# Kernel optimization log

Hardware: AMD Instinct MI355X
Metric: run time of the kernel (lower is better)

Reference implementation:

```python
import jax, jax.numpy as jnp
import numpy as np

NEG_SLOPE = 0.01  # nn.LeakyReLU default

def leaky_relu(x):
    return jnp.where(x >= 0, x, NEG_SLOPE * x)

B, C, H, W = 256, 256, 5, 5
L = H * W          # 25 locations (h==5 so no adaptive pooling)
D = C + 1          # +1 coordinate feature
HID = 64
OUT_UNITS = 32

def setup_inputs() -> dict:
    key = jax.random.key(0)
    ks = jax.random.split(key, 9)
    def xavier(k, shape):
        fan_out, fan_in = shape
        a = np.sqrt(6.0 / (fan_in + fan_out))
        return jax.random.uniform(k, shape, jnp.float32, -a, a)
    return {
        "x_img": jax.random.normal(ks[0], (B, C, H, W), jnp.float32),
        "g0_w": xavier(ks[1], (HID, 2 * D)),
        "g0_b": jnp.zeros((HID,), jnp.float32),
        "g1_w": xavier(ks[2], (HID, HID)),
        "g1_b": jnp.zeros((HID,), jnp.float32),
        "post_w": xavier(ks[3], (HID, HID)),
        "post_b": jnp.zeros((HID,), jnp.float32),
        "out_w": xavier(ks[4], (OUT_UNITS, HID)),
        "out_b": jnp.zeros((OUT_UNITS,), jnp.float32),
        "num_step": 0,
    }

def reference(x_img, g0_w, g0_b, g1_w, g1_b, post_w, post_b, out_w, out_b, num_step):
    b, c, h, w = x_img.shape
    length = h * w
    # (b, c, h*w) -> (b, L, c)
    feats = x_img.reshape(b, c, length).transpose(0, 2, 1)
    # append coordinate index feature
    coords = jnp.broadcast_to(jnp.arange(length, dtype=x_img.dtype)[None, :, None], (b, length, 1))
    feats = jnp.concatenate([feats, coords], axis=2)          # (b, L, D)
    d = feats.shape[-1]
    # all-pairs concat: x_i varies over axis 2, x_j over axis 1 (matches torch repeat/cat order)
    x_i = jnp.broadcast_to(feats[:, None, :, :], (b, length, length, d))
    x_j = jnp.broadcast_to(feats[:, :, None, :], (b, length, length, d))
    pair = jnp.concatenate([x_i, x_j], axis=3)                 # (b, L, L, 2D)
    # per-pair MLP g
    out = leaky_relu(jnp.einsum('blmd,kd->blmk', pair, g0_w) + g0_b)
    out = leaky_relu(jnp.einsum('blmk,jk->blmj', out, g1_w) + g1_b)
    # reduce over both pair axes
    out = out.sum(axis=(1, 2))                                 # (b, HID)
    # f
    out = leaky_relu(out @ post_w.T + post_b)
    out = leaky_relu(out @ out_w.T + out_b)                    # (b, OUT_UNITS)
    return out
```

## Files before the change

### kernel.cpp

```cpp
#include <hip/hip_runtime.h>

#define NB 256
#define NC 256
#define NL 25
#define ND 257
#define NOUT 32

__device__ __forceinline__ float lrelu(float x) {
    return fmaxf(x, 0.0f) + 0.01f * fminf(x, 0.0f);
}

__global__ void k_transpose(const float* __restrict__ g0, float* __restrict__ wt) {
    __shared__ float tile[64][65];
    const int cbase = blockIdx.x * 64;
    const int jh = blockIdx.y;
    const int tid = threadIdx.x;
    for (int i = tid; i < 64 * 64; i += 256) {
        int r = i >> 6, cc = i & 63, c = cbase + cc;
        float v = 0.0f;
        if (c < ND) v = g0[r * (2 * ND) + jh * ND + c];
        tile[r][cc] = v;
    }
    __syncthreads();
    for (int i = tid; i < 64 * 64; i += 256) {
        int cc = i >> 6, r = i & 63, c = cbase + cc;
        if (c < ND) wt[c * 128 + jh * 64 + r] = tile[r][cc];
    }
}

__global__ __launch_bounds__(512, 4)
void k_main(const float* __restrict__ x_img,
            const float* __restrict__ wt,
            const float* __restrict__ g0_b,
            const float* __restrict__ g1_w,
            const float* __restrict__ g1_b,
            const float* __restrict__ post_w,
            const float* __restrict__ post_b,
            const float* __restrict__ out_w,
            const float* __restrict__ out_b,
            float* __restrict__ out)
{
    __shared__ __align__(16) float xsu[6400];
    __shared__ __align__(16) float Pb[6400];
    __shared__ __align__(16) float b0s[64];
    float* xs  = xsu;
    float* uvl = xsu;
    float* red = xsu + 3200;
    float* zs  = xsu + 3520;
    float* sf  = xsu + 3584;

    const int tid  = threadIdx.x;
    const int b    = blockIdx.x;
    const int lane = tid & 63;
    const int wid  = tid >> 6;

    {
        const float4* src = (const float4*)(x_img + (size_t)b * (NC * NL));
        float4* dst = (float4*)xs;
        for (int i = tid; i < 1600; i += 512) dst[i] = src[i];
    }
    if (tid < 64) b0s[tid] = g0_b[tid];
    __syncthreads();

    {
        const int r     = tid & 255;
        const int chalf = tid >> 8;
        const int k4    = r & 15;
        const int uv    = (r >> 4) & 1;
        const int pgrp  = r >> 5;
        const int pstart = pgrp * 3;
        const bool p4   = (pgrp == 7);
        float4 a0 = {0.f,0.f,0.f,0.f}, a1 = a0, a2 = a0, a3 = a0;
        const float4* wp = ((const float4*)wt) + (uv * 16 + k4);
        const float* xrow = xs + pstart;
        const int c0   = chalf ? 128 : 0;
        const int cend = chalf ? 256 : 128;
        #pragma unroll 2
        for (int c = c0; c < cend; ++c) {
            const float4 w4 = wp[c * 32];
            const float f0 = xrow[c * 25 + 0];
            const float f1 = xrow[c * 25 + 1];
            const float f2 = xrow[c * 25 + 2];
            a0.x = fmaf(w4.x, f0, a0.x); a0.y = fmaf(w4.y, f0, a0.y);
            a0.z = fmaf(w4.z, f0, a0.z); a0.w = fmaf(w4.w, f0, a0.w);
            a1.x = fmaf(w4.x, f1, a1.x); a1.y = fmaf(w4.y, f1, a1.y);
            a1.z = fmaf(w4.z, f1, a1.z); a1.w = fmaf(w4.w, f1, a1.w);
            a2.x = fmaf(w4.x, f2, a2.x); a2.y = fmaf(w4.y, f2, a2.y);
            a2.z = fmaf(w4.z, f2, a2.z); a2.w = fmaf(w4.w, f2, a2.w);
            if (p4) {
                const float f3 = xrow[c * 25 + 3];
                a3.x = fmaf(w4.x, f3, a3.x); a3.y = fmaf(w4.y, f3, a3.y);
                a3.z = fmaf(w4.z, f3, a3.z); a3.w = fmaf(w4.w, f3, a3.w);
            }
        }
        if (chalf) {
            const float4 w4 = wp[256 * 32];
            const float f0 = (float)(pstart + 0);
            const float f1 = (float)(pstart + 1);
            const float f2 = (float)(pstart + 2);
            a0.x = fmaf(w4.x, f0, a0.x); a0.y = fmaf(w4.y, f0, a0.y);
            a0.z = fmaf(w4.z, f0, a0.z); a0.w = fmaf(w4.w, f0, a0.w);
            a1.x = fmaf(w4.x, f1, a1.x); a1.y = fmaf(w4.y, f1, a1.y);
            a1.z = fmaf(w4.z, f1, a1.z); a1.w = fmaf(w4.w, f1, a1.w);
            a2.x = fmaf(w4.x, f2, a2.x); a2.y = fmaf(w4.y, f2, a2.y);
            a2.z = fmaf(w4.z, f2, a2.z); a2.w = fmaf(w4.w, f2, a2.w);
            if (p4) {
                const float f3 = (float)(pstart + 3);
                a3.x = fmaf(w4.x, f3, a3.x); a3.y = fmaf(w4.y, f3, a3.y);
                a3.z = fmaf(w4.z, f3, a3.z); a3.w = fmaf(w4.w, f3, a3.w);
            }
        }
        float* dst = Pb + (chalf * 2 + uv) * 1600;
        *(float4*)&dst[(pstart + 0) * 64 + k4 * 4] = a0;
        *(float4*)&dst[(pstart + 1) * 64 + k4 * 4] = a1;
        *(float4*)&dst[(pstart + 2) * 64 + k4 * 4] = a2;
        if (p4) *(float4*)&dst[(pstart + 3) * 64 + k4 * 4] = a3;
    }
    __syncthreads();

    for (int i = tid; i < 800; i += 512) {
        const int uv  = i >= 400;
        const int rem = i - uv * 400;
        const int p   = rem >> 4;
        const int k4  = rem & 15;
        const float4 pa = *(const float4*)&Pb[uv * 1600 + p * 64 + k4 * 4];
        const float4 pc = *(const float4*)&Pb[(2 + uv) * 1600 + p * 64 + k4 * 4];
        float4 o;
        o.x = pa.x + pc.x; o.y = pa.y + pc.y;
        o.z = pa.z + pc.z; o.w = pa.w + pc.w;
        if (!uv) {
            o.x += b0s[k4 * 4 + 0]; o.y += b0s[k4 * 4 + 1];
            o.z += b0s[k4 * 4 + 2]; o.w += b0s[k4 * 4 + 3];
        }
        *(float4*)&uvl[uv * 1600 + p * 64 + ((k4 ^ (p & 15)) << 2)] = o;
    }
    __syncthreads();

    const int pg = wid >> 1;
    const int jb = __builtin_amdgcn_readfirstlane((wid & 1) * 32);
    const float* __restrict__ gbase = g1_w + (size_t)jb * 64;

    float accS[32];
    #pragma unroll
    for (int q = 0; q < 32; ++q) accS[q] = 0.f;

    #pragma unroll 1
    for (int batch = pg; batch < 10; batch += 4) {
        const int pp0 = batch * 64 + lane;
        const bool ok = pp0 < 625;
        const int pp = ok ? pp0 : 624;
        const int l = (pp * 5243) >> 17;
        const int m = pp - l * 25;
        const int ub = m * 64;          const int usw = m & 15;
        const int vb = 1600 + l * 64;   const int vsw = l & 15;

        float dot[32];
        #pragma unroll
        for (int q = 0; q < 32; ++q) dot[q] = 0.f;

        #pragma unroll 2
        for (int kc = 0; kc < 16; ++kc) {
            const float4 u4 = *(const float4*)&uvl[ub + ((kc ^ usw) << 2)];
            const float4 v4 = *(const float4*)&uvl[vb + ((kc ^ vsw) << 2)];
            float4 h;
            h.x = lrelu(u4.x + v4.x);
            h.y = lrelu(u4.y + v4.y);
            h.z = lrelu(u4.z + v4.z);
            h.w = lrelu(u4.w + v4.w);
            #pragma unroll
            for (int q = 0; q < 32; ++q) {
                const float4 g4 = *(const float4*)(gbase + q * 64 + kc * 4);
                dot[q] = fmaf(g4.x, h.x, dot[q]);
                dot[q] = fmaf(g4.y, h.y, dot[q]);
                dot[q] = fmaf(g4.z, h.z, dot[q]);
                dot[q] = fmaf(g4.w, h.w, dot[q]);
            }
        }
        #pragma unroll
        for (int q = 0; q < 32; ++q) {
            const float t = lrelu(dot[q] + g1_b[jb + q]);
            accS[q] += ok ? t : 0.0f;
        }
    }

    {
        float vout = 0.f;
        #pragma unroll
        for (int q = 0; q < 32; ++q) {
            float s = accS[q];
            s += __shfl_xor(s, 1, 64);
            s += __shfl_xor(s, 2, 64);
            s += __shfl_xor(s, 4, 64);
            s += __shfl_xor(s, 8, 64);
            s += __shfl_xor(s, 16, 64);
            s += __shfl_xor(s, 32, 64);
            vout = (lane == q) ? s : vout;
        }
        if (lane < 32) red[(jb + lane) * 5 + pg] = vout;
    }
    __syncthreads();

    if (tid < 64) {
        const float* rp = red + tid * 5;
        sf[tid] = ((rp[0] + rp[1]) + (rp[2] + rp[3]));
        float a = post_b[tid];
        #pragma unroll 8
        for (int k = 0; k < 64; ++k) a = fmaf(post_w[tid * 64 + k], sf[k], a);
        zs[tid] = lrelu(a);
        if (tid < NOUT) {
            float a2 = out_b[tid];
            #pragma unroll 8
            for (int k = 0; k < 64; ++k) a2 = fmaf(out_w[tid * 64 + k], zs[k], a2);
            out[b * NOUT + tid] = lrelu(a2);
        }
    }
}

extern "C" void kernel_launch(void* const* d_in, const int* in_sizes, int n_in,
                              void* d_out, int out_size, void* d_ws, size_t ws_size,
                              hipStream_t stream) {
    const float* x_img  = (const float*)d_in[0];
    const float* g0_w   = (const float*)d_in[1];
    const float* g0_b   = (const float*)d_in[2];
    const float* g1_w   = (const float*)d_in[3];
    const float* g1_b   = (const float*)d_in[4];
    const float* post_w = (const float*)d_in[5];
    const float* post_b = (const float*)d_in[6];
    const float* out_w  = (const float*)d_in[7];
    const float* out_b  = (const float*)d_in[8];
    float* out = (float*)d_out;
    float* wt  = (float*)d_ws;

    k_transpose<<<dim3(5, 2), 256, 0, stream>>>(g0_w, wt);
    k_main<<<NB, 512, 0, stream>>>(x_img, wt, g0_b, g1_w, g1_b,
                                   post_w, post_b, out_w, out_b, out);
}
```

Before: 171.3 us.

## Split each batch's pair work across three blocks and add post-MLP kernel

The main kernel now launches three blocks per batch item. Each block handles a subset of the 10 pair batches (4, 3 or 3) and writes a partial 64-wide sum to workspace. A new small kernel adds the three partials and runs the post and output MLP layers. The goal is to fill more of the GPU's compute units, since 256 blocks is fewer than the CU count times occupancy allows. The cost is that each of the three blocks redoes the x load and the first-layer projection, plus one more kernel launch. LeakyReLU is also simplified to a single fmax.

Result: no change. 170.8 us (-0.3%).

```diff
diff --git a/kernel.cpp b/kernel.cpp
--- a/kernel.cpp
+++ b/kernel.cpp
@@ -6,8 +6,11 @@
 #define ND 257
 #define NOUT 32
 
+#define WS_WT 0
+#define WS_S  32896
+
 __device__ __forceinline__ float lrelu(float x) {
-    return fmaxf(x, 0.0f) + 0.01f * fminf(x, 0.0f);
+    return fmaxf(x, 0.01f * x);
 }
 
 __global__ void k_transpose(const float* __restrict__ g0, float* __restrict__ wt) {
@@ -34,11 +37,7 @@
             const float* __restrict__ g0_b,
             const float* __restrict__ g1_w,
             const float* __restrict__ g1_b,
-            const float* __restrict__ post_w,
-            const float* __restrict__ post_b,
-            const float* __restrict__ out_w,
-            const float* __restrict__ out_b,
-            float* __restrict__ out)
+            float* __restrict__ wsS)
 {
     __shared__ __align__(16) float xsu[6400];
     __shared__ __align__(16) float Pb[6400];
@@ -46,11 +45,11 @@
     float* xs  = xsu;
     float* uvl = xsu;
     float* red = xsu + 3200;
-    float* zs  = xsu + 3520;
-    float* sf  = xsu + 3584;
 
     const int tid  = threadIdx.x;
-    const int b    = blockIdx.x;
+    const unsigned bid = blockIdx.x;
+    const int b    = (int)(bid / 3u);
+    const int h    = (int)(bid - 3u * b);
     const int lane = tid & 63;
     const int wid  = tid >> 6;
 
@@ -136,6 +135,8 @@
     }
     __syncthreads();
 
+    const int start = (h == 0) ? 0 : (3 * h + 1);
+    const int count = (h == 0) ? 4 : 3;
     const int pg = wid >> 1;
     const int jb = __builtin_amdgcn_readfirstlane((wid & 1) * 32);
     const float* __restrict__ gbase = g1_w + (size_t)jb * 64;
@@ -144,8 +145,8 @@
     #pragma unroll
     for (int q = 0; q < 32; ++q) accS[q] = 0.f;
 
-    #pragma unroll 1
-    for (int batch = pg; batch < 10; batch += 4) {
+    if (pg < count) {
+        const int batch = start + pg;
         const int pp0 = batch * 64 + lane;
         const bool ok = pp0 < 625;
         const int pp = ok ? pp0 : 624;
@@ -162,18 +163,18 @@
         for (int kc = 0; kc < 16; ++kc) {
             const float4 u4 = *(const float4*)&uvl[ub + ((kc ^ usw) << 2)];
             const float4 v4 = *(const float4*)&uvl[vb + ((kc ^ vsw) << 2)];
-            float4 h;
-            h.x = lrelu(u4.x + v4.x);
-            h.y = lrelu(u4.y + v4.y);
-            h.z = lrelu(u4.z + v4.z);
-            h.w = lrelu(u4.w + v4.w);
+            float4 hh;
+            hh.x = lrelu(u4.x + v4.x);
+            hh.y = lrelu(u4.y + v4.y);
+            hh.z = lrelu(u4.z + v4.z);
+            hh.w = lrelu(u4.w + v4.w);
             #pragma unroll
             for (int q = 0; q < 32; ++q) {
                 const float4 g4 = *(const float4*)(gbase + q * 64 + kc * 4);
-                dot[q] = fmaf(g4.x, h.x, dot[q]);
-                dot[q] = fmaf(g4.y, h.y, dot[q]);
-                dot[q] = fmaf(g4.z, h.z, dot[q]);
-                dot[q] = fmaf(g4.w, h.w, dot[q]);
+                dot[q] = fmaf(g4.x, hh.x, dot[q]);
+                dot[q] = fmaf(g4.y, hh.y, dot[q]);
+                dot[q] = fmaf(g4.z, hh.z, dot[q]);
+                dot[q] = fmaf(g4.w, hh.w, dot[q]);
             }
         }
         #pragma unroll
@@ -202,17 +203,30 @@
 
     if (tid < 64) {
         const float* rp = red + tid * 5;
-        sf[tid] = ((rp[0] + rp[1]) + (rp[2] + rp[3]));
-        float a = post_b[tid];
+        wsS[(size_t)b * 192 + h * 64 + tid] = (rp[0] + rp[1]) + (rp[2] + rp[3]);
+    }
+}
+
+__global__ __launch_bounds__(64)
+void k_post(const float* __restrict__ wsS, const float* __restrict__ post_w,
+            const float* __restrict__ post_b, const float* __restrict__ out_w,
+            const float* __restrict__ out_b, float* __restrict__ out)
+{
+    __shared__ float ss[64], zs[64];
+    const int b = blockIdx.x, tid = threadIdx.x;
+    const float* sp = wsS + (size_t)b * 192;
+    ss[tid] = sp[tid] + sp[64 + tid] + sp[128 + tid];
+    __syncthreads();
+    float a = post_b[tid];
+    #pragma unroll 8
+    for (int k = 0; k < 64; ++k) a = fmaf(post_w[tid * 64 + k], ss[k], a);
+    zs[tid] = lrelu(a);
+    __syncthreads();
+    if (tid < NOUT) {
+        float a2 = out_b[tid];
         #pragma unroll 8
-        for (int k = 0; k < 64; ++k) a = fmaf(post_w[tid * 64 + k], sf[k], a);
-        zs[tid] = lrelu(a);
-        if (tid < NOUT) {
-            float a2 = out_b[tid];
-            #pragma unroll 8
-            for (int k = 0; k < 64; ++k) a2 = fmaf(out_w[tid * 64 + k], zs[k], a2);
-            out[b * NOUT + tid] = lrelu(a2);
-        }
+        for (int k = 0; k < 64; ++k) a2 = fmaf(out_w[tid * 64 + k], zs[k], a2);
+        out[b * NOUT + tid] = lrelu(a2);
     }
 }
 
@@ -229,9 +243,9 @@
     const float* out_w  = (const float*)d_in[7];
     const float* out_b  = (const float*)d_in[8];
     float* out = (float*)d_out;
-    float* wt  = (float*)d_ws;
-
-    k_transpose<<<dim3(5, 2), 256, 0, stream>>>(g0_w, wt);
-    k_main<<<NB, 512, 0, stream>>>(x_img, wt, g0_b, g1_w, g1_b,
-                                   post_w, post_b, out_w, out_b, out);
-}
+    float* ws  = (float*)d_ws;
+
+    k_transpose<<<dim3(5, 2), 256, 0, stream>>>(g0_w, ws + WS_WT);
+    k_main<<<NB * 3, 512, 0, stream>>>(x_img, ws + WS_WT, g0_b, g1_w, g1_b, ws + WS_S);
+    k_post<<<NB, 64, 0, stream>>>(ws + WS_S, post_w, post_b, out_w, out_b, out);
+}
```
